# Performance work log

Hardware: AMD Instinct MI355X
Metric: run time of the kernel (lower is better)

Reference implementation:

```python
import jax, jax.numpy as jnp
import numpy as np

DELTA = 1e-6  # small constant used throughout the original repo


def _theta(memory, keys):
    # batchwise cosine similarity: memory [b,m,w], keys [b,r,w] -> [b,r,m]
    a = memory / (jnp.linalg.norm(memory, axis=2, keepdims=True) + DELTA)
    b = keys / (jnp.linalg.norm(keys, axis=2, keepdims=True) + DELTA)
    return jnp.einsum('bmw,brw->brm', a, b)


def _content_weightings(memory, keys, strengths):
    d = _theta(memory, keys)                       # [b,r,m]
    s = jax.nn.softplus(strengths)[..., None]      # [b,r,1]
    return jax.nn.softmax(d * s, axis=2)


def _allocate(usage):
    # usage [b,m]
    u = DELTA + (1.0 - DELTA) * usage
    phi = jnp.argsort(u, axis=1)                          # ascending, like topk(largest=False)
    sorted_u = jnp.take_along_axis(u, phi, axis=1)
    sorted_alloc = (1.0 - sorted_u) * jnp.cumprod(sorted_u, axis=1)  # fake_cumprod == inclusive cumprod
    alloc = jnp.take_along_axis(sorted_alloc, phi, axis=1)           # faithful to .gather(1, phi) in source
    return alloc[:, None, :]                              # [b,1,m]


def _dnc_step(xi, W, bW, memory, link_matrix, precedence, read_weights, write_weights, usage_vector):
    b, m, w = memory.shape
    r = read_weights.shape[1]
    iface = xi @ W + bW                                   # [b, r*w + 3*w + 5*r + 3]
    i0 = r * w
    read_keys = iface[:, :i0].reshape(b, r, w)
    read_strengths = 1.0 + jax.nn.relu(iface[:, i0:i0 + r])              # [b,r]
    write_key = iface[:, i0 + r:i0 + r + w].reshape(b, 1, w)
    write_strength = (1.0 + jax.nn.relu(iface[:, i0 + r + w]))[:, None]  # [b,1]
    erase_vector = jax.nn.sigmoid(iface[:, i0 + r + w + 1:i0 + r + 2 * w + 1]).reshape(b, 1, w)
    write_vector = iface[:, i0 + r + 2 * w + 1:i0 + r + 3 * w + 1].reshape(b, 1, w)
    free_gates = jax.nn.sigmoid(iface[:, i0 + r + 3 * w + 1:i0 + 2 * r + 3 * w + 1])  # [b,r]
    allocation_gate = jax.nn.sigmoid(iface[:, i0 + 2 * r + 3 * w + 1])[:, None]       # [b,1]
    write_gate = jax.nn.sigmoid(iface[:, i0 + 2 * r + 3 * w + 2])[:, None]            # [b,1]
    # NOTE: source slices read_modes starting at the write_gate index (faithful) and softmaxes over dim 1
    read_modes = jax.nn.softmax(iface[:, i0 + 2 * r + 3 * w + 2:i0 + 5 * r + 3 * w + 2].reshape(b, r, 3), axis=1)

    # ---- write path ----
    usage = usage_vector + (1.0 - usage_vector) * (1.0 - jnp.prod(1.0 - write_weights, axis=1))
    psi = jnp.prod(1.0 - free_gates[:, :, None] * read_weights, axis=1)  # [b,m]
    usage = usage * psi

    write_content_w = _content_weightings(memory, write_key, write_strength)  # [b,1,m]
    alloc = _allocate(usage)                                                  # [b,1,m]
    ag = allocation_gate[:, :, None]
    wg = write_gate[:, :, None]
    new_write_w = wg * (ag * alloc + (1.0 - ag) * write_content_w)            # [b,1,m]

    weighted_resets = new_write_w[:, :, :, None] * erase_vector[:, :, None, :]  # [b,1,m,w]
    reset_gate = jnp.prod(1.0 - weighted_resets, axis=1)                        # [b,m,w]
    new_memory = memory * reset_gate + jnp.einsum('bkm,bkw->bmw', new_write_w, write_vector)

    prec4 = precedence[:, :, None, :]            # [b,1,1,m]
    ww_i = new_write_w[:, :, :, None]            # [b,1,m,1]
    ww_j = new_write_w[:, :, None, :]            # [b,1,1,m]
    new_link = (1.0 - ww_i - ww_j) * link_matrix + ww_i * prec4
    new_link = new_link * (1.0 - jnp.eye(m, dtype=memory.dtype))[None, None]

    new_prec = (1.0 - jnp.sum(new_write_w, axis=2, keepdims=True)) * precedence + new_write_w

    # ---- read path ----
    content_w = _content_weightings(new_memory, read_keys, read_strengths)  # [b,r,m]
    forward_w = jnp.einsum('bkmn,brn->brkm', new_link, read_weights)        # [b,r,1,m]
    backward_w = jnp.einsum('brm,bkmn->brkn', read_weights, new_link)       # [b,r,1,m]
    content_mode = read_modes[:, :, 2:3] * content_w
    backward_mode = jnp.sum(read_modes[:, :, 0:1, None] * backward_w, axis=2)
    forward_mode = jnp.sum(read_modes[:, :, 1:2, None] * forward_w, axis=2)
    new_read_w = backward_mode + content_mode + forward_mode                # [b,r,m]

    read_vectors = jnp.einsum('brm,bmw->brw', new_read_w, new_memory)       # [b,r,w]
    return read_vectors


def setup_inputs() -> dict:
    key = jax.random.key(0)
    ks = jax.random.split(key, 3)
    b, m, w, r, d = 64, 1024, 64, 4, 512
    iface_size = r * w + 3 * w + 5 * r + 3  # 471
    return {
        'xi': jax.random.normal(ks[0], (b, d), dtype=jnp.float32),
        'W': jax.random.normal(ks[1], (d, iface_size), dtype=jnp.float32) * 0.05,
        'bW': jnp.zeros((iface_size,), dtype=jnp.float32),
        'memory': jnp.zeros((b, m, w), dtype=jnp.float32),
        'link_matrix': jnp.zeros((b, 1, m, m), dtype=jnp.float32),
        'precedence': jnp.zeros((b, 1, m), dtype=jnp.float32),
        'read_weights': jnp.zeros((b, r, m), dtype=jnp.float32),
        'write_weights': jnp.zeros((b, 1, m), dtype=jnp.float32),
        'usage_vector': jnp.zeros((b, m), dtype=jnp.float32),
    }


def reference(xi, W, bW, memory, link_matrix, precedence, read_weights, write_weights, usage_vector):
    return _dnc_step(xi, W, bW, memory, link_matrix, precedence, read_weights, write_weights, usage_vector)
```

## Files before the change

kernel.cpp:

```cpp
#include <hip/hip_runtime.h>

#define DELTA 1e-6f

#define NB 64
#define NM 1024
#define NW 64
#define NR 4
#define ND 512
#define NIF 471

typedef unsigned long long ull;

__device__ __forceinline__ float sigmoidf_(float x){ return 1.0f/(1.0f+expf(-x)); }
__device__ __forceinline__ float softplusf_(float x){ return fmaxf(x,0.0f) + log1pf(expf(-fabsf(x))); }

__device__ __forceinline__ float waveSum(float v){
  #pragma unroll
  for(int o=32;o>0;o>>=1) v += __shfl_down(v,o,64);
  return v;
}
__device__ __forceinline__ float waveMax(float v){
  #pragma unroll
  for(int o=32;o>0;o>>=1) v = fmaxf(v, __shfl_down(v,o,64));
  return v;
}
__device__ __forceinline__ ull shflxor64(ull k, int m){
  unsigned lo = (unsigned)(k & 0xffffffffu), hi = (unsigned)(k>>32);
  lo = (unsigned)__shfl_xor((int)lo, m, 64);
  hi = (unsigned)__shfl_xor((int)hi, m, 64);
  return ((ull)hi<<32)|lo;
}

__global__ __launch_bounds__(256) void k_iface(const float* __restrict__ xi,
                                               const float* __restrict__ Wm,
                                               const float* __restrict__ bW,
                                               float* __restrict__ iface,
                                               float4* __restrict__ out4){
  int b = blockIdx.x, half = blockIdx.y;
  __shared__ float xs[ND];
  if (half == 0 && threadIdx.x < 64) out4[b*64 + threadIdx.x] = make_float4(0.f,0.f,0.f,0.f);
  for(int k=threadIdx.x;k<ND;k+=256) xs[k]=xi[b*ND+k];
  __syncthreads();
  int c = half*236 + threadIdx.x;
  int cend = half ? NIF : 236;
  if (c < cend){
    float acc = bW[c];
    #pragma unroll 4
    for(int k=0;k<ND;k++) acc = fmaf(xs[k], Wm[k*NIF+c], acc);
    iface[b*NIF+c]=acc;
  }
}

__global__ __launch_bounds__(256) void k_wcos(
    const float* __restrict__ iface, const float* __restrict__ mem,
    const float* __restrict__ rw_old, const float* __restrict__ ww_old,
    const float* __restrict__ uv,
    float* __restrict__ uu, float* __restrict__ wcd, float* __restrict__ wcn){
  int b = blockIdx.y;
  int j = blockIdx.x*256 + threadIdx.x;
  __shared__ float wkey[NW];
  const float* ifb = iface + b*NIF;
  if (threadIdx.x < NW) wkey[threadIdx.x] = ifb[260+threadIdx.x];
  __syncthreads();
  float fg0=sigmoidf_(ifb[453]), fg1=sigmoidf_(ifb[454]);
  float fg2=sigmoidf_(ifb[455]), fg3=sigmoidf_(ifb[456]);
  float u0  = uv[b*NM+j];
  float wwo = ww_old[b*NM+j];
  float usage = u0 + (1.0f-u0)*wwo;
  float psi = (1.0f - fg0*rw_old[(b*NR+0)*NM+j])
            * (1.0f - fg1*rw_old[(b*NR+1)*NM+j])
            * (1.0f - fg2*rw_old[(b*NR+2)*NM+j])
            * (1.0f - fg3*rw_old[(b*NR+3)*NM+j]);
  usage *= psi;
  uu[b*NM+j] = DELTA + (1.0f-DELTA)*usage;
  float dot=0.0f, nrm=0.0f;
  const float4* mrow4 = (const float4*)(mem + ((size_t)b*NM + j)*NW);
  #pragma unroll 4
  for(int k=0;k<16;k++){
    float4 mv = mrow4[k];
    const float* wk = wkey + k*4;
    dot = fmaf(mv.x,wk[0],dot); dot = fmaf(mv.y,wk[1],dot);
    dot = fmaf(mv.z,wk[2],dot); dot = fmaf(mv.w,wk[3],dot);
    nrm = fmaf(mv.x,mv.x,nrm); nrm = fmaf(mv.y,mv.y,nrm);
    nrm = fmaf(mv.z,mv.z,nrm); nrm = fmaf(mv.w,mv.w,nrm);
  }
  wcd[b*NM+j]=dot; wcn[b*NM+j]=nrm;
}

__global__ __launch_bounds__(1024) void k_write2(
    const float* __restrict__ iface, const float* __restrict__ uu,
    const float* __restrict__ wcd, const float* __restrict__ wcn,
    float* __restrict__ wwp, float* __restrict__ sPK){
  int b = blockIdx.x; int tid = threadIdx.x;
  int lane = tid & 63, wv = tid >> 6;
  __shared__ float wkey[NW];
  __shared__ ull skA[NM];
  __shared__ ull skB[NM];
  __shared__ float fb2[NM];
  __shared__ float red[17];
  __shared__ float s_wp[16], s_wp2[16];
  const float* ifb = iface + b*NIF;
  if (tid < NW) wkey[tid] = ifb[260+tid];
  if (tid < 16) sPK[b*16+tid] = 0.0f;
  __syncthreads();
  float sw = softplusf_(1.0f + fmaxf(ifb[324],0.0f));
  float ag = sigmoidf_(ifb[457]);
  float wg = sigmoidf_(ifb[458]);
  float kn=0.0f;
  for(int k=0;k<NW;k++){ float t=wkey[k]; kn += t*t; }
  kn = sqrtf(kn);
  float logit = sw * wcd[b*NM+tid] / ((sqrtf(wcn[b*NM+tid])+DELTA)*(kn+DELTA));
  float m1 = waveMax(logit); if(lane==0) red[wv]=m1; __syncthreads();
  if(tid==0){ float mm=red[0]; for(int i=1;i<16;i++) mm=fmaxf(mm,red[i]); red[16]=mm; } __syncthreads();
  float e = expf(logit - red[16]);
  float s1 = waveSum(e); if(lane==0) red[wv]=s1; __syncthreads();
  if(tid==0){ float ss=0; for(int i=0;i<16;i++) ss+=red[i]; red[16]=ss; } __syncthreads();
  float wcw = e/red[16];
  float u = uu[b*NM+tid];
  ull k = ((ull)__float_as_uint(u) << 32) | (unsigned)tid;
  bool useA = true;
  for (int k2=2; k2<=NM; k2<<=1){
    for (int jj=k2>>1; jj>0; jj>>=1){
      ull p;
      if (jj >= 64){
        ull* buf = useA ? skA : skB;
        buf[tid] = k;
        __syncthreads();
        p = buf[tid^jj];
        useA = !useA;
      } else {
        p = shflxor64(k, jj);
      }
      bool lower = (tid & jj) == 0;
      bool asc   = (tid & k2) == 0;
      bool takeMin = (lower == asc);
      k = takeMin ? (k<p ? k : p) : (k>p ? k : p);
    }
  }
  float su = __uint_as_float((unsigned)(k>>32));
  int phi  = (int)(k & 0xffffffffu);
  float sc = su;
  #pragma unroll
  for (int off=1; off<64; off<<=1){
    float t = __shfl_up(sc, off, 64);
    if (lane >= off) sc *= t;
  }
  if (lane==63) s_wp[wv] = sc;
  __syncthreads();
  if (tid==0){
    float p=1.0f;
    for (int w=0;w<16;w++){ float t=s_wp[w]; s_wp2[w]=p; p*=t; }
  }
  __syncthreads();
  float P = sc * s_wp2[wv];
  float salloc = (1.0f - su)*P;
  fb2[phi] = salloc;
  __syncthreads();
  float alloc = fb2[tid];
  wwp[b*NM+tid] = wg*(ag*alloc + (1.0f-ag)*wcw);
}

__global__ __launch_bounds__(256) void k_link8(
    const float* __restrict__ link, const float* __restrict__ rw,
    const float* __restrict__ wwp,
    float4* __restrict__ RFp, float* __restrict__ C2p, float* __restrict__ C3p,
    float* __restrict__ ldiag){
  int cx = blockIdx.x, ry = blockIdx.y, b = blockIdx.z;
  int tid = threadIdx.x, lane = tid&63, wv = tid>>6;
  __shared__ float4 s_L4[32*64];
  __shared__ float4 s_gcol4[256];
  __shared__ float  s_mwc[256];
  __shared__ float4 s_grow4[32];
  __shared__ float  s_wwr[32];
  __shared__ float4 s_rfp4[128];
  const float* Lb = link + ((size_t)b<<20);
  int colbase = cx*256, rowbase = ry*256;
  {
    float g0 = rw[(b*NR+0)*NM + colbase + tid];
    float g1 = rw[(b*NR+1)*NM + colbase + tid];
    float g2 = rw[(b*NR+2)*NM + colbase + tid];
    float g3 = rw[(b*NR+3)*NM + colbase + tid];
    s_gcol4[tid] = make_float4(g0,g1,g2,g3);
    s_mwc[tid] = 1.0f - wwp[b*NM + colbase + tid];
  }
  float c2a[NR][4], c3a[NR][4];
  #pragma unroll
  for(int r=0;r<NR;r++){
    #pragma unroll
    for(int e=0;e<4;e++){ c2a[r][e]=0.0f; c3a[r][e]=0.0f; }
  }
  for (int ch=0; ch<8; ++ch){
    int rb = rowbase + ch*32;
    if (tid < 128) ((float*)s_grow4)[tid] = rw[(b*NR+(tid&3))*NM + rb + (tid>>2)];
    if (tid < 32)  s_wwr[tid] = wwp[b*NM + rb + tid];
    #pragma unroll
    for (int jq=0;jq<8;jq++){
      int rl = wv + 4*jq;
      float4 lv = *(const float4*)(Lb + (size_t)(rb+rl)*NM + colbase + lane*4);
      s_L4[rl*64 + (lane ^ ((rl>>1)&7))] = lv;
    }
    __syncthreads();
    if (cx == ry && tid < 32){
      int coff = ch*32 + tid;
      float4 v = s_L4[tid*64 + ((coff>>2) ^ ((tid>>1)&7))];
      float d = (coff&1) ? ((coff&2)? v.w : v.y) : ((coff&2)? v.z : v.x);
      ldiag[b*NM + rb + tid] = d;
    }
    {
      int i5 = lane & 15, cg = lane >> 4;
      int rl0 = 2*i5;
      int sz = i5 & 7;
      float wwj0 = s_wwr[rl0], wwj1 = s_wwr[rl0+1];
      float rf0[4] = {0,0,0,0}, rf1[4] = {0,0,0,0};
      #pragma unroll
      for (int q=0;q<4;q++){
        int cq = wv*16 + cg*4 + q;
        float4 mw  = ((const float4*)s_mwc)[cq];
        float4 lv0 = s_L4[rl0*64 + (cq ^ sz)];
        float4 lv1 = s_L4[(rl0+1)*64 + (cq ^ sz)];
        float le0[4]={lv0.x,lv0.y,lv0.z,lv0.w};
        float le1[4]={lv1.x,lv1.y,lv1.z,lv1.w};
        float mv[4]={mw.x,mw.y,mw.z,mw.w};
        #pragma unroll
        for (int e=0;e<4;e++){
          float4 gv = s_gcol4[cq*4+e];
          float lt0 = le0[e]*(mv[e]-wwj0);
          float lt1 = le1[e]*(mv[e]-wwj1);
          rf0[0]=fmaf(lt0,gv.x,rf0[0]); rf0[1]=fmaf(lt0,gv.y,rf0[1]);
          rf0[2]=fmaf(lt0,gv.z,rf0[2]); rf0[3]=fmaf(lt0,gv.w,rf0[3]);
          rf1[0]=fmaf(lt1,gv.x,rf1[0]); rf1[1]=fmaf(lt1,gv.y,rf1[1]);
          rf1[2]=fmaf(lt1,gv.z,rf1[2]); rf1[3]=fmaf(lt1,gv.w,rf1[3]);
        }
      }
      #pragma unroll
      for (int r=0;r<NR;r++){
        rf0[r] += __shfl_xor(rf0[r], 16, 64);
        rf0[r] += __shfl_xor(rf0[r], 32, 64);
        rf1[r] += __shfl_xor(rf1[r], 16, 64);
        rf1[r] += __shfl_xor(rf1[r], 32, 64);
      }
      if (cg == 0){
        s_rfp4[wv*32 + rl0]     = make_float4(rf0[0],rf0[1],rf0[2],rf0[3]);
        s_rfp4[wv*32 + rl0 + 1] = make_float4(rf1[0],rf1[1],rf1[2],rf1[3]);
      }
    }
    #pragma unroll 2
    for (int ri=0; ri<8; ri++){
      int row = wv*8 + ri;
      float4 lv = s_L4[row*64 + (lane ^ ((row>>1)&7))];
      float4 gg = s_grow4[row];
      float wwr = s_wwr[row];
      float le[4] = {lv.x,lv.y,lv.z,lv.w};
      float ggv[4] = {gg.x,gg.y,gg.z,gg.w};
      float ggw[4];
      #pragma unroll
      for (int r=0;r<NR;r++) ggw[r] = ggv[r]*wwr;
      #pragma unroll
      for (int e=0;e<4;e++){
        #pragma unroll
        for (int r=0;r<NR;r++){
          c2a[r][e] = fmaf(le[e], ggv[r], c2a[r][e]);
          c3a[r][e] = fmaf(le[e], ggw[r], c3a[r][e]);
        }
      }
    }
    __syncthreads();
    if (tid < 128){
      int row = tid>>2, r = tid&3;
      float s = ((const float*)&s_rfp4[0*32+row])[r] + ((const float*)&s_rfp4[1*32+row])[r]
              + ((const float*)&s_rfp4[2*32+row])[r] + ((const float*)&s_rfp4[3*32+row])[r];
      ((float*)RFp)[((size_t)cx<<18) + (b*NM + rb + row)*4 + r] = s;
    }
    __syncthreads();
  }
  float4* s_comb = s_L4;
  #pragma unroll
  for (int r=0;r<NR;r++){
    s_comb[tid*8 + r]     = make_float4(c2a[r][0],c2a[r][1],c2a[r][2],c2a[r][3]);
    s_comb[tid*8 + 4 + r] = make_float4(c3a[r][0],c3a[r][1],c3a[r][2],c3a[r][3]);
  }
  __syncthreads();
  for (int t=tid; t<512; t+=256){
    int lc = t>>3, q = t&7;
    float4 a = s_comb[(0*64+lc)*8+q];
    float4 bb= s_comb[(1*64+lc)*8+q];
    float4 c = s_comb[(2*64+lc)*8+q];
    float4 d = s_comb[(3*64+lc)*8+q];
    float4 s = make_float4(a.x+bb.x+c.x+d.x, a.y+bb.y+c.y+d.y, a.z+bb.z+c.z+d.z, a.w+bb.w+c.w+d.w);
    float* dst = (q<4) ? &C2p[((size_t)ry<<18) + (b*NR+q)*NM + colbase + lc*4]
                       : &C3p[((size_t)ry<<18) + (b*NR+(q-4))*NM + colbase + lc*4];
    *(float4*)dst = s;
  }
}

__global__ __launch_bounds__(256) void k_rdots2(
    const float* __restrict__ iface, const float* __restrict__ mem,
    const float* __restrict__ wwp, const float* __restrict__ prec,
    const float* __restrict__ rw_old,
    float* __restrict__ ce, float* __restrict__ sPK){
  int b = blockIdx.y, jt = blockIdx.x;
  int tid = threadIdx.x, lane = tid&63, wv = tid>>6;
  __shared__ float keys[NR][NW];
  __shared__ float er[NW], wvec[NW];
  __shared__ float sk[NR];
  __shared__ float red[4][12];
  const float* ifb = iface + b*NIF;
  { int r=tid>>6, kk=tid&63; keys[r][kk] = ifb[r*NW+kk]; }
  if (tid < 64) er[tid] = sigmoidf_(ifb[325+tid]);
  else if (tid < 128) wvec[tid-64] = ifb[389+tid-64];
  else if (tid < 132){
    int r = tid-128;
    float knv=0;
    for(int k=0;k<NW;k++){ float t=ifb[r*NW+k]; knv += t*t; }
    sk[r] = softplusf_(1.0f + fmaxf(ifb[256+r],0.0f)) / (sqrtf(knv)+DELTA);
  }
  __syncthreads();
  int j = jt*256 + tid;
  float wwj = wwp[b*NM+j];
  float pj  = prec[b*NM+j];
  const float* mrow = mem + ((size_t)b*NM+j)*NW;
  float dt[NR]={0,0,0,0}; float nrm=0.0f;
  for(int k=0;k<NW;k++){
    float nmv = fmaf(mrow[k], (1.0f - wwj*er[k]), wwj*wvec[k]);
    nrm = fmaf(nmv,nmv,nrm);
    #pragma unroll
    for(int r=0;r<NR;r++) dt[r] = fmaf(nmv, keys[r][k], dt[r]);
  }
  float inv = 1.0f/(sqrtf(nrm)+DELTA);
  float v12[12];
  #pragma unroll
  for(int r=0;r<NR;r++){
    float e = expf(sk[r]*dt[r]*inv);
    ce[(b*NR+r)*NM + j] = e;
    float rwv = rw_old[(b*NR+r)*NM+j];
    v12[r]   = pj*rwv;
    v12[4+r] = wwj*rwv;
    v12[8+r] = e;
  }
  #pragma unroll
  for(int q=0;q<12;q++){
    float s = waveSum(v12[q]);
    if (lane==0) red[wv][q] = s;
  }
  __syncthreads();
  if (tid < 12){
    float s = red[0][tid]+red[1][tid]+red[2][tid]+red[3][tid];
    atomicAdd(&sPK[b*16+tid], s);
  }
}

__global__ __launch_bounds__(256) void k_readf(
    const float* __restrict__ iface, const float* __restrict__ mem,
    const float* __restrict__ wwp, const float* __restrict__ prec,
    const float* __restrict__ rw_old, const float* __restrict__ ldiag,
    const float4* __restrict__ RFp4, const float* __restrict__ C2p, const float* __restrict__ C3p,
    const float* __restrict__ ce, const float* __restrict__ sPK,
    float* __restrict__ out){
  int jt = blockIdx.x, b = blockIdx.y;
  int tid = threadIdx.x, lane = tid&63, wv = tid>>6;
  __shared__ float s_nrw[NR][256];
  __shared__ float s_ww[256];
  __shared__ float s_er[NW], s_wv[NW];
  __shared__ float s_acc[4][NR][NW];
  __shared__ float rm[NR][3];
  __shared__ float s_sc[16];
  const float* ifb = iface + b*NIF;
  if (tid == 0){
    for(int mo=0;mo<3;mo++){
      float x0=ifb[458+0*3+mo], x1=ifb[458+1*3+mo], x2=ifb[458+2*3+mo], x3=ifb[458+3*3+mo];
      float mx = fmaxf(fmaxf(x0,x1),fmaxf(x2,x3));
      float e0=expf(x0-mx),e1=expf(x1-mx),e2=expf(x2-mx),e3=expf(x3-mx);
      float s=e0+e1+e2+e3;
      rm[0][mo]=e0/s; rm[1][mo]=e1/s; rm[2][mo]=e2/s; rm[3][mo]=e3/s;
    }
  }
  if (tid >= 64 && tid < 80)  s_sc[tid-64] = sPK[b*16 + (tid-64)];
  if (tid >= 128 && tid < 192) s_er[tid-128] = sigmoidf_(ifb[325+tid-128]);
  if (tid >= 192)              s_wv[tid-192] = ifb[389+tid-192];
  int j0 = jt*256;
  int j = j0 + tid;
  float wwj = wwp[b*NM+j];
  s_ww[tid] = wwj;
  __syncthreads();
  float pj  = prec[b*NM+j];
  float Ljj = ldiag[b*NM+j];
  float4 Fa = RFp4[(0<<16) + b*NM + j];
  float4 Fb = RFp4[(1<<16) + b*NM + j];
  float4 Fc = RFp4[(2<<16) + b*NM + j];
  float4 Fd = RFp4[(3<<16) + b*NM + j];
  float Fr[4] = {Fa.x+Fb.x+Fc.x+Fd.x, Fa.y+Fb.y+Fc.y+Fd.y,
                 Fa.z+Fb.z+Fc.z+Fd.z, Fa.w+Fb.w+Fc.w+Fd.w};
  #pragma unroll
  for(int r=0;r<NR;r++){
    int idx = (b*NR+r)*NM + j;
    float cc2 = C2p[idx] + C2p[262144+idx] + C2p[524288+idx] + C2p[786432+idx];
    float cc3 = C3p[idx] + C3p[262144+idx] + C3p[524288+idx] + C3p[786432+idx];
    float grj = rw_old[idx];
    float cwv = ce[idx] / s_sc[8+r];
    float fwd = Fr[r] - Ljj*grj*(1.0f-2.0f*wwj) + wwj*(s_sc[r] - pj*grj);
    float bwd = (cc2 - cc3) - Ljj*grj*(1.0f-wwj) - wwj*(cc2 - Ljj*grj) + pj*(s_sc[4+r] - wwj*grj);
    s_nrw[r][tid] = rm[r][0]*bwd + rm[r][1]*fwd + rm[r][2]*cwv;
  }
  __syncthreads();
  int w = lane;
  float erw = s_er[w], wvw = s_wv[w];
  float acc[NR]={0,0,0,0};
  for(int jj=0;jj<64;jj++){
    int jl = wv*64+jj;
    float wwr = s_ww[jl];
    float nmv = fmaf(mem[((size_t)b*NM + j0+jl)*NW + w], (1.0f - wwr*erw), wwr*wvw);
    #pragma unroll
    for(int r=0;r<NR;r++) acc[r] = fmaf(s_nrw[r][jl], nmv, acc[r]);
  }
  #pragma unroll
  for(int r=0;r<NR;r++) s_acc[wv][r][w] = acc[r];
  __syncthreads();
  {
    int r = tid>>6, k = tid&63;
    float s = s_acc[0][r][k]+s_acc[1][r][k]+s_acc[2][r][k]+s_acc[3][r][k];
    atomicAdd(&out[b*NR*NW + r*NW + k], s);
  }
}

extern "C" void kernel_launch(void* const* d_in, const int* in_sizes, int n_in,
                              void* d_out, int out_size, void* d_ws, size_t ws_size,
                              hipStream_t stream) {
  (void)in_sizes; (void)n_in; (void)out_size; (void)ws_size;
  const float* xi   = (const float*)d_in[0];
  const float* Wm   = (const float*)d_in[1];
  const float* bW   = (const float*)d_in[2];
  const float* mem  = (const float*)d_in[3];
  const float* link = (const float*)d_in[4];
  const float* prec = (const float*)d_in[5];
  const float* rw   = (const float*)d_in[6];
  const float* wwo  = (const float*)d_in[7];
  const float* uv   = (const float*)d_in[8];
  float* out = (float*)d_out;
  float* ws  = (float*)d_ws;
  float* iface = ws;
  float* wwp   = ws + 30208;
  float* uu    = ws + 95744;
  float* wcd   = ws + 161280;
  float* wcn   = ws + 226816;
  float* ce    = ws + 292352;
  float* ldiag = ws + 554496;
  float* sPK   = ws + 620032;
  float* RFp   = ws + 621056;
  float* C2p   = ws + 1669632;
  float* C3p   = ws + 2718208;
  k_iface<<<dim3(NB,2), 256, 0, stream>>>(xi, Wm, bW, iface, (float4*)out);
  k_wcos <<<dim3(4,NB), 256, 0, stream>>>(iface, mem, rw, wwo, uv, uu, wcd, wcn);
  k_write2<<<NB, 1024, 0, stream>>>(iface, uu, wcd, wcn, wwp, sPK);
  k_link8<<<dim3(4,4,NB), 256, 0, stream>>>(link, rw, wwp, (float4*)RFp, C2p, C3p, ldiag);
  k_rdots2<<<dim3(4,NB), 256, 0, stream>>>(iface, mem, wwp, prec, rw, ce, sPK);
  k_readf<<<dim3(4,NB), 256, 0, stream>>>(iface, mem, wwp, prec, rw, ldiag,
                                          (const float4*)RFp, C2p, C3p, ce, sPK, out);
}
```

Before: 149.0 us.

## Merge iface/wcos and link/rdots kernels via block-role dispatch

Folds the interface GEMV and the write-content cosine kernel into one launch: extra blocks recompute the write key and free gates they need directly from xi and W, so they no longer wait on the iface kernel. It also folds the read-dots kernel into the link kernel as an extra grid row that reuses the link kernel's shared memory. Both changes cut the launch count from six to four and let independent work run concurrently. The cost is redundant GEMV columns computed per block and heavier shared-memory use for the dot blocks.

Measured after the change: 153.3 us. 1.03x slower.

```diff
diff --git a/kernel.cpp b/kernel.cpp
--- a/kernel.cpp
+++ b/kernel.cpp
@@ -31,39 +31,47 @@
   return ((ull)hi<<32)|lo;
 }
 
-__global__ __launch_bounds__(256) void k_iface(const float* __restrict__ xi,
-                                               const float* __restrict__ Wm,
-                                               const float* __restrict__ bW,
-                                               float* __restrict__ iface,
-                                               float4* __restrict__ out4){
-  int b = blockIdx.x, half = blockIdx.y;
+__global__ __launch_bounds__(256) void k_ifw(
+    const float* __restrict__ xi, const float* __restrict__ Wm, const float* __restrict__ bW,
+    const float* __restrict__ mem, const float* __restrict__ rw_old,
+    const float* __restrict__ ww_old, const float* __restrict__ uv,
+    float* __restrict__ iface, float4* __restrict__ out4,
+    float* __restrict__ uu, float* __restrict__ wcd, float* __restrict__ wcn){
+  int role = blockIdx.x, b = blockIdx.y;
+  int tid = threadIdx.x;
   __shared__ float xs[ND];
-  if (half == 0 && threadIdx.x < 64) out4[b*64 + threadIdx.x] = make_float4(0.f,0.f,0.f,0.f);
-  for(int k=threadIdx.x;k<ND;k+=256) xs[k]=xi[b*ND+k];
-  __syncthreads();
-  int c = half*236 + threadIdx.x;
-  int cend = half ? NIF : 236;
-  if (c < cend){
+  __shared__ float wkey[NW];
+  __shared__ float fgs[4];
+  for(int k=tid;k<ND;k+=256) xs[k]=xi[b*ND+k];
+  if (role == 0 && tid < 64) out4[b*64 + tid] = make_float4(0.f,0.f,0.f,0.f);
+  __syncthreads();
+  if (role < 2){
+    int c = role*236 + tid;
+    int cend = role ? NIF : 236;
+    if (c < cend){
+      float acc = bW[c];
+      #pragma unroll 4
+      for(int k=0;k<ND;k++) acc = fmaf(xs[k], Wm[k*NIF+c], acc);
+      iface[b*NIF+c]=acc;
+    }
+    return;
+  }
+  if (tid < 64){
+    int c = 260 + tid;
     float acc = bW[c];
     #pragma unroll 4
     for(int k=0;k<ND;k++) acc = fmaf(xs[k], Wm[k*NIF+c], acc);
-    iface[b*NIF+c]=acc;
-  }
-}
-
-__global__ __launch_bounds__(256) void k_wcos(
-    const float* __restrict__ iface, const float* __restrict__ mem,
-    const float* __restrict__ rw_old, const float* __restrict__ ww_old,
-    const float* __restrict__ uv,
-    float* __restrict__ uu, float* __restrict__ wcd, float* __restrict__ wcn){
-  int b = blockIdx.y;
-  int j = blockIdx.x*256 + threadIdx.x;
-  __shared__ float wkey[NW];
-  const float* ifb = iface + b*NIF;
-  if (threadIdx.x < NW) wkey[threadIdx.x] = ifb[260+threadIdx.x];
-  __syncthreads();
-  float fg0=sigmoidf_(ifb[453]), fg1=sigmoidf_(ifb[454]);
-  float fg2=sigmoidf_(ifb[455]), fg3=sigmoidf_(ifb[456]);
+    wkey[tid] = acc;
+  } else if (tid < 68){
+    int c = 453 + (tid-64);
+    float acc = bW[c];
+    #pragma unroll 4
+    for(int k=0;k<ND;k++) acc = fmaf(xs[k], Wm[k*NIF+c], acc);
+    fgs[tid-64] = sigmoidf_(acc);
+  }
+  __syncthreads();
+  int j = (role-2)*256 + tid;
+  float fg0=fgs[0], fg1=fgs[1], fg2=fgs[2], fg3=fgs[3];
   float u0  = uv[b*NM+j];
   float wwo = ww_old[b*NM+j];
   float usage = u0 + (1.0f-u0)*wwo;
@@ -160,19 +168,78 @@
   wwp[b*NM+tid] = wg*(ag*alloc + (1.0f-ag)*wcw);
 }
 
-__global__ __launch_bounds__(256) void k_link8(
+__global__ __launch_bounds__(256) void k_linkdots(
     const float* __restrict__ link, const float* __restrict__ rw,
     const float* __restrict__ wwp,
     float4* __restrict__ RFp, float* __restrict__ C2p, float* __restrict__ C3p,
-    float* __restrict__ ldiag){
-  int cx = blockIdx.x, ry = blockIdx.y, b = blockIdx.z;
+    float* __restrict__ ldiag,
+    const float* __restrict__ iface, const float* __restrict__ mem,
+    const float* __restrict__ prec, const float* __restrict__ rw_old,
+    float* __restrict__ ce, float* __restrict__ sPK){
   int tid = threadIdx.x, lane = tid&63, wv = tid>>6;
+  int b = blockIdx.z;
   __shared__ float4 s_L4[32*64];
   __shared__ float4 s_gcol4[256];
   __shared__ float  s_mwc[256];
   __shared__ float4 s_grow4[32];
   __shared__ float  s_wwr[32];
   __shared__ float4 s_rfp4[128];
+
+  if (blockIdx.y == 4){
+    float* base = (float*)s_L4;
+    float* keys = base;
+    float* er   = base + 256;
+    float* wvec = base + 320;
+    float* sk   = base + 384;
+    float* red  = base + 392;
+    int jt = blockIdx.x;
+    const float* ifb = iface + b*NIF;
+    { int r=tid>>6, kk=tid&63; keys[r*NW+kk] = ifb[r*NW+kk]; }
+    if (tid < 64) er[tid] = sigmoidf_(ifb[325+tid]);
+    else if (tid < 128) wvec[tid-64] = ifb[389+tid-64];
+    else if (tid < 132){
+      int r = tid-128;
+      float knv=0;
+      for(int k=0;k<NW;k++){ float t=ifb[r*NW+k]; knv += t*t; }
+      sk[r] = softplusf_(1.0f + fmaxf(ifb[256+r],0.0f)) / (sqrtf(knv)+DELTA);
+    }
+    __syncthreads();
+    int j = jt*256 + tid;
+    float wwj = wwp[b*NM+j];
+    float pj  = prec[b*NM+j];
+    const float* mrow = mem + ((size_t)b*NM+j)*NW;
+    float dt[NR]={0,0,0,0}; float nrm=0.0f;
+    for(int k=0;k<NW;k++){
+      float nmv = fmaf(mrow[k], (1.0f - wwj*er[k]), wwj*wvec[k]);
+      nrm = fmaf(nmv,nmv,nrm);
+      #pragma unroll
+      for(int r=0;r<NR;r++) dt[r] = fmaf(nmv, keys[r*NW+k], dt[r]);
+    }
+    float inv = 1.0f/(sqrtf(nrm)+DELTA);
+    float v12[12];
+    #pragma unroll
+    for(int r=0;r<NR;r++){
+      float e = expf(sk[r]*dt[r]*inv);
+      ce[(b*NR+r)*NM + j] = e;
+      float rwv = rw_old[(b*NR+r)*NM+j];
+      v12[r]   = pj*rwv;
+      v12[4+r] = wwj*rwv;
+      v12[8+r] = e;
+    }
+    #pragma unroll
+    for(int q=0;q<12;q++){
+      float s = waveSum(v12[q]);
+      if (lane==0) red[wv*12+q] = s;
+    }
+    __syncthreads();
+    if (tid < 12){
+      float s = red[0*12+tid]+red[1*12+tid]+red[2*12+tid]+red[3*12+tid];
+      atomicAdd(&sPK[b*16+tid], s);
+    }
+    return;
+  }
+
+  int cx = blockIdx.x, ry = blockIdx.y;
   const float* Lb = link + ((size_t)b<<20);
   int colbase = cx*256, rowbase = ry*256;
   {
@@ -293,62 +360,6 @@
   }
 }
 
-__global__ __launch_bounds__(256) void k_rdots2(
-    const float* __restrict__ iface, const float* __restrict__ mem,
-    const float* __restrict__ wwp, const float* __restrict__ prec,
-    const float* __restrict__ rw_old,
-    float* __restrict__ ce, float* __restrict__ sPK){
-  int b = blockIdx.y, jt = blockIdx.x;
-  int tid = threadIdx.x, lane = tid&63, wv = tid>>6;
-  __shared__ float keys[NR][NW];
-  __shared__ float er[NW], wvec[NW];
-  __shared__ float sk[NR];
-  __shared__ float red[4][12];
-  const float* ifb = iface + b*NIF;
-  { int r=tid>>6, kk=tid&63; keys[r][kk] = ifb[r*NW+kk]; }
-  if (tid < 64) er[tid] = sigmoidf_(ifb[325+tid]);
-  else if (tid < 128) wvec[tid-64] = ifb[389+tid-64];
-  else if (tid < 132){
-    int r = tid-128;
-    float knv=0;
-    for(int k=0;k<NW;k++){ float t=ifb[r*NW+k]; knv += t*t; }
-    sk[r] = softplusf_(1.0f + fmaxf(ifb[256+r],0.0f)) / (sqrtf(knv)+DELTA);
-  }
-  __syncthreads();
-  int j = jt*256 + tid;
-  float wwj = wwp[b*NM+j];
-  float pj  = prec[b*NM+j];
-  const float* mrow = mem + ((size_t)b*NM+j)*NW;
-  float dt[NR]={0,0,0,0}; float nrm=0.0f;
-  for(int k=0;k<NW;k++){
-    float nmv = fmaf(mrow[k], (1.0f - wwj*er[k]), wwj*wvec[k]);
-    nrm = fmaf(nmv,nmv,nrm);
-    #pragma unroll
-    for(int r=0;r<NR;r++) dt[r] = fmaf(nmv, keys[r][k], dt[r]);
-  }
-  float inv = 1.0f/(sqrtf(nrm)+DELTA);
-  float v12[12];
-  #pragma unroll
-  for(int r=0;r<NR;r++){
-    float e = expf(sk[r]*dt[r]*inv);
-    ce[(b*NR+r)*NM + j] = e;
-    float rwv = rw_old[(b*NR+r)*NM+j];
-    v12[r]   = pj*rwv;
-    v12[4+r] = wwj*rwv;
-    v12[8+r] = e;
-  }
-  #pragma unroll
-  for(int q=0;q<12;q++){
-    float s = waveSum(v12[q]);
-    if (lane==0) red[wv][q] = s;
-  }
-  __syncthreads();
-  if (tid < 12){
-    float s = red[0][tid]+red[1][tid]+red[2][tid]+red[3][tid];
-    atomicAdd(&sPK[b*16+tid], s);
-  }
-}
-
 __global__ __launch_bounds__(256) void k_readf(
     const float* __restrict__ iface, const float* __restrict__ mem,
     const float* __restrict__ wwp, const float* __restrict__ prec,
@@ -448,11 +459,11 @@
   float* RFp   = ws + 621056;
   float* C2p   = ws + 1669632;
   float* C3p   = ws + 2718208;
-  k_iface<<<dim3(NB,2), 256, 0, stream>>>(xi, Wm, bW, iface, (float4*)out);
-  k_wcos <<<dim3(4,NB), 256, 0, stream>>>(iface, mem, rw, wwo, uv, uu, wcd, wcn);
+  k_ifw  <<<dim3(6,NB), 256, 0, stream>>>(xi, Wm, bW, mem, rw, wwo, uv,
+                                          iface, (float4*)out, uu, wcd, wcn);
   k_write2<<<NB, 1024, 0, stream>>>(iface, uu, wcd, wcn, wwp, sPK);
-  k_link8<<<dim3(4,4,NB), 256, 0, stream>>>(link, rw, wwp, (float4*)RFp, C2p, C3p, ldiag);
-  k_rdots2<<<dim3(4,NB), 256, 0, stream>>>(iface, mem, wwp, prec, rw, ce, sPK);
+  k_linkdots<<<dim3(4,5,NB), 256, 0, stream>>>(link, rw, wwp, (float4*)RFp, C2p, C3p, ldiag,
+                                               iface, mem, prec, rw, ce, sPK);
   k_readf<<<dim3(4,NB), 256, 0, stream>>>(iface, mem, wwp, prec, rw, ldiag,
                                           (const float4*)RFp, C2p, C3p, ce, sPK, out);
 }
```
